# Kernel optimization log

Hardware: AMD Instinct MI355X
Metric: run time of the kernel (lower is better)

Reference implementation:

```python
import jax, jax.numpy as jnp
import numpy as np

B, D_IN, M, D_MEM = 65536, 64, 2048, 64


def setup_inputs() -> dict:
    key = jax.random.key(0)
    k = jax.random.split(key, 5)
    glorot = lambda kk, shape: jax.random.uniform(
        kk, shape, jnp.float32,
        -jnp.sqrt(6.0 / (shape[0] + shape[1])), jnp.sqrt(6.0 / (shape[0] + shape[1])))
    return {
        "inputs": jax.random.normal(k[0], (B, D_IN), jnp.float32),
        "W_att": glorot(k[1], (D_IN, M)),
        "b_att": jnp.zeros((M,), jnp.float32),
        "W_write": glorot(k[2], (D_IN, D_MEM)),
        "b_write": jnp.zeros((D_MEM,), jnp.float32),
        "memory": glorot(k[3], (M, D_MEM)),
        "update_gate": jnp.full((M,), 0.5, jnp.float32),
    }


def reference(inputs, W_att, b_att, W_write, b_write, memory, update_gate):
    # Read attention: Dense(memory_size, softmax) -> [B, M]
    read_attention = jax.nn.softmax(inputs @ W_att + b_att, axis=-1)
    # Read: [B, M] @ [M, Dm] -> [B, Dm]
    read_vector = read_attention @ memory
    # Write candidate: Dense(memory_dim, tanh) -> [B, Dm]
    candidate_write = jnp.tanh(inputs @ W_write + b_write)
    aggregated_write = jnp.mean(candidate_write, axis=0)[None, :]  # [1, Dm]
    write_attention = jnp.mean(read_attention, axis=0)             # [M]
    update_weights = (write_attention * update_gate)[:, None]      # [M, 1]
    # Gated in-place memory update (returned as new state)
    new_memory = memory * (1.0 - update_weights) + update_weights * aggregated_write
    return read_vector, new_memory
```

## Files before the change

kernel.cpp:

```cpp
#include <hip/hip_runtime.h>
#include <hip/hip_bf16.h>

typedef unsigned int   u32;
typedef unsigned short u16;

typedef __bf16 bf16x8 __attribute__((ext_vector_type(8)));
typedef float  f32x4  __attribute__((ext_vector_type(4)));
typedef u32    u32x4  __attribute__((ext_vector_type(4)));

union Frag { u32x4 u; bf16x8 b; };

#define MFMA16 __builtin_amdgcn_mfma_f32_16x16x32_bf16

#define B_ROWS 65536
#define D_IN   64
#define M_SZ   2048
#define D_MEM  64

#define WT_OFF      0
#define MEMT_OFF    262144
#define WWT_OFF     524288
#define CSF_OFF     532480
#define AGF_OFF     540672
#define CSP_OFF     540928
#define AGP_OFF     8929536
#define WS_REQUIRED 9191680

#define L2E 1.4426950408889634f

__device__ __forceinline__ float bf2f(u16 h) { return __uint_as_float(((u32)h) << 16); }
__device__ __forceinline__ u16 f2bf(float f) {
    u32 u = __float_as_uint(f);
    return (u16)((u + 0x7FFFu + ((u >> 16) & 1u)) >> 16);
}
__device__ __forceinline__ u16 f2bf_fast(float f) {
    return (u16)((__float_as_uint(f) + 0x8000u) >> 16);
}
#if defined(__has_builtin) && __has_builtin(__builtin_amdgcn_exp2f)
__device__ __forceinline__ float exp2fast(float x) { return __builtin_amdgcn_exp2f(x); }
#else
__device__ __forceinline__ float exp2fast(float x) { return __expf(x * 0.6931471805599453f); }
#endif
__device__ __forceinline__ float tanh_fast(float x) {
    const float e = exp2fast(x * (2.0f * L2E));
    return 1.0f - 2.0f * __builtin_amdgcn_rcpf(e + 1.0f);
}
__device__ __forceinline__ bool detect_bf16(const void* ug) {
    return ((const u32*)ug)[0] == 0x3F003F00u;
}
__device__ __forceinline__ float load_elem(const void* p, size_t i, bool isbf) {
    return isbf ? bf2f(((const u16*)p)[i]) : ((const float*)p)[i];
}

__global__ void __launch_bounds__(256)
prep_kernel(const void* Watt, const void* mem_in, const void* Wwr, const void* ug,
            u16* Wt, u16* memT, u16* Wwt, float* CSF)
{
    const bool isbf = detect_bf16(ug);
    const int b = blockIdx.x;
    const int t = threadIdx.x;
    if (b == 65) {
        for (int i = t; i < 2112; i += 256) CSF[i] = 0.f;
        return;
    }
    __shared__ u16 tile[64][65];
    const void* src; u16* dst; int R, C, rb, cb;
    if (b < 32)      { src = Watt;   dst = Wt;   R = 64;   C = 2048; rb = 0;           cb = b * 64; }
    else if (b < 64) { src = mem_in; dst = memT; R = 2048; C = 64;   rb = (b-32) * 64; cb = 0;      }
    else             { src = Wwr;    dst = Wwt;  R = 64;   C = 64;   rb = 0;           cb = 0;      }

#pragma unroll
    for (int j = 0; j < 16; ++j) {
        int e = j * 256 + t;
        int r = e >> 6, c = e & 63;
        float v = load_elem(src, (size_t)(rb + r) * C + cb + c, isbf);
        tile[r][c] = f2bf(v);
    }
    __syncthreads();
#pragma unroll
    for (int j = 0; j < 16; ++j) {
        int e = j * 256 + t;
        int c2 = e >> 6, r2 = e & 63;
        dst[(size_t)(cb + c2) * R + rb + r2] = tile[r2][c2];
    }
}

__global__ void __launch_bounds__(256, 2)
main_kernel(const void* x_in, const void* batt_in, const void* bwrite_in,
            const u16* __restrict__ Wt, const u16* __restrict__ memT,
            const u16* __restrict__ Wwt, const void* ug,
            float* CSF, float* AGF, u16* cs_part, u16* ag_part,
            int use_part, void* out)
{
    const bool isbf = detect_bf16(ug);
    const int tid = threadIdx.x;
    const int lane = tid & 63, wave = tid >> 6;
    const int quad = lane >> 4, l4 = lane & 15;
    const int rowbase = blockIdx.x * 128;
    const int wrow = blockIdx.x * 4 + wave;

    __shared__ __align__(16) u16 WtL[2][64][72];
    __shared__ __align__(16) u16 MeL[2][64][72];
    __shared__ __align__(16) u16 P[4][32][72];
    __shared__ float battL[2048];

    {
        const int i0 = tid * 8;
#pragma unroll
        for (int j = 0; j < 8; ++j)
            battL[i0 + j] = load_elem(batt_in, i0 + j, isbf) * L2E;
    }

    const int srow = tid >> 2, sg = (tid & 3) * 16;
    auto stageWt = [&](int c, int b) {
        const u16* g = Wt + ((size_t)c * 64 + srow) * 64 + sg;
        u32x4 v0 = *(const u32x4*)g;
        u32x4 v1 = *(const u32x4*)(g + 8);
        *(u32x4*)&WtL[b][srow][sg]     = v0;
        *(u32x4*)&WtL[b][srow][sg + 8] = v1;
    };
    auto stageMe = [&](int c, int b) {
        const u16* g = memT + (size_t)srow * 2048 + c * 64 + sg;
        u32x4 v0 = *(const u32x4*)g;
        u32x4 v1 = *(const u32x4*)(g + 8);
        *(u32x4*)&MeL[b][srow][sg]     = v0;
        *(u32x4*)&MeL[b][srow][sg + 8] = v1;
    };

    Frag a[2][2];
#pragma unroll
    for (int rg = 0; rg < 2; ++rg) {
        const int arow = rowbase + wave * 32 + rg * 16 + l4;
        if (isbf) {
            const u16* xp = (const u16*)x_in + (size_t)arow * 64 + quad * 8;
            a[rg][0].u = *(const u32x4*)xp;
            a[rg][1].u = *(const u32x4*)(xp + 32);
        } else {
            const float* xp = (const float*)x_in + (size_t)arow * 64 + quad * 8;
#pragma unroll
            for (int j = 0; j < 8; ++j) {
                ((u16*)&a[rg][0])[j] = f2bf(xp[j]);
                ((u16*)&a[rg][1])[j] = f2bf(xp[32 + j]);
            }
        }
    }
    const f32x4 zf = {0.f, 0.f, 0.f, 0.f};

    stageWt(0, 0);

    float agout = 0.f;
    {
        f32x4 accW[4][2];
#pragma unroll
        for (int t = 0; t < 4; ++t) {
            const u16* bp = Wwt + (size_t)(t * 16 + l4) * 64 + quad * 8;
            Frag b0, b1; b0.u = *(const u32x4*)bp; b1.u = *(const u32x4*)(bp + 32);
#pragma unroll
            for (int rg = 0; rg < 2; ++rg) {
                accW[t][rg] = MFMA16(a[rg][0].b, b0.b, zf, 0, 0, 0);
                accW[t][rg] = MFMA16(a[rg][1].b, b1.b, accW[t][rg], 0, 0, 0);
            }
        }
#pragma unroll
        for (int t = 0; t < 4; ++t) {
            const float bw = load_elem(bwrite_in, t * 16 + l4, isbf);
            float s = 0.f;
#pragma unroll
            for (int rg = 0; rg < 2; ++rg)
#pragma unroll
                for (int i = 0; i < 4; ++i) s += tanh_fast(accW[t][rg][i] + bw);
            s += __shfl_xor(s, 16, 64);
            s += __shfl_xor(s, 32, 64);
            if (quad == t) agout = s;
        }
    }
    if (use_part) ag_part[wrow * 64 + lane] = f2bf(agout);
    else          atomicAdd(&AGF[lane], agout);

    __syncthreads();

    float lr[2][4] = {{0.f,0.f,0.f,0.f},{0.f,0.f,0.f,0.f}};
    for (int c = 0; c < 32; ++c) {
        const int buf = c & 1;
        if (c < 31) stageWt(c + 1, buf ^ 1);
        const int mbase = c * 64;
        Frag wb0[4], wb1[4]; float bl[4];
#pragma unroll
        for (int t = 0; t < 4; ++t) {
            wb0[t].u = *(const u32x4*)&WtL[buf][t * 16 + l4][quad * 8];
            wb1[t].u = *(const u32x4*)&WtL[buf][t * 16 + l4][32 + quad * 8];
            bl[t] = battL[mbase + t * 16 + l4];
        }
#pragma unroll
        for (int t = 0; t < 4; ++t)
#pragma unroll
            for (int rg = 0; rg < 2; ++rg) {
                f32x4 acc = MFMA16(a[rg][0].b, wb0[t].b, zf, 0, 0, 0);
                acc = MFMA16(a[rg][1].b, wb1[t].b, acc, 0, 0, 0);
#pragma unroll
                for (int i = 0; i < 4; ++i)
                    lr[rg][i] += exp2fast(fmaf(acc[i], L2E, bl[t]));
            }
        __syncthreads();
    }
#pragma unroll
    for (int rg = 0; rg < 2; ++rg)
#pragma unroll
        for (int i = 0; i < 4; ++i) {
            float v = lr[rg][i];
            v += __shfl_xor(v, 1, 64); v += __shfl_xor(v, 2, 64);
            v += __shfl_xor(v, 4, 64); v += __shfl_xor(v, 8, 64);
            lr[rg][i] = 1.f / v;
        }

    f32x4 oacc[2][4] = {{zf,zf,zf,zf},{zf,zf,zf,zf}};
    stageWt(0, 0); stageMe(0, 0);
    __syncthreads();
    for (int c = 0; c < 32; ++c) {
        const int buf = c & 1;
        if (c < 31) { stageWt(c + 1, buf ^ 1); stageMe(c + 1, buf ^ 1); }
        const int mbase = c * 64;
        Frag wb0[4], wb1[4], mb0[4], mb1[4]; float bl[4];
#pragma unroll
        for (int t = 0; t < 4; ++t) {
            wb0[t].u = *(const u32x4*)&WtL[buf][t * 16 + l4][quad * 8];
            wb1[t].u = *(const u32x4*)&WtL[buf][t * 16 + l4][32 + quad * 8];
            bl[t] = battL[mbase + t * 16 + l4];
            mb0[t].u = *(const u32x4*)&MeL[buf][t * 16 + l4][quad * 8];
            mb1[t].u = *(const u32x4*)&MeL[buf][t * 16 + l4][32 + quad * 8];
        }
        float cst[4];
#pragma unroll
        for (int t = 0; t < 4; ++t) {
            float cs = 0.f;
#pragma unroll
            for (int rg = 0; rg < 2; ++rg) {
                f32x4 acc = MFMA16(a[rg][0].b, wb0[t].b, zf, 0, 0, 0);
                acc = MFMA16(a[rg][1].b, wb1[t].b, acc, 0, 0, 0);
#pragma unroll
                for (int i = 0; i < 4; ++i) {
                    const float e = exp2fast(fmaf(acc[i], L2E, bl[t]));
                    const float p = e * lr[rg][i];
                    cs += p;
                    P[wave][rg * 16 + quad * 4 + i][t * 16 + l4] = f2bf_fast(p);
                }
            }
            cst[t] = cs;
        }
        Frag ap[2][2];
#pragma unroll
        for (int rg = 0; rg < 2; ++rg) {
            ap[rg][0].u = *(const u32x4*)&P[wave][rg * 16 + l4][quad * 8];
            ap[rg][1].u = *(const u32x4*)&P[wave][rg * 16 + l4][32 + quad * 8];
        }
#pragma unroll
        for (int dt = 0; dt < 4; ++dt)
#pragma unroll
            for (int rg = 0; rg < 2; ++rg) {
                oacc[rg][dt] = MFMA16(ap[rg][0].b, mb0[dt].b, oacc[rg][dt], 0, 0, 0);
                oacc[rg][dt] = MFMA16(ap[rg][1].b, mb1[dt].b, oacc[rg][dt], 0, 0, 0);
            }
        float csout = 0.f;
#pragma unroll
        for (int t = 0; t < 4; ++t) {
            float v = cst[t];
            v += __shfl_xor(v, 16, 64);
            v += __shfl_xor(v, 32, 64);
            if (quad == t) csout = v;
        }
        if (use_part) cs_part[(size_t)wrow * 2048 + mbase + lane] = f2bf(csout);
        else          atomicAdd(&CSF[mbase + lane], csout);
        __syncthreads();
    }

#pragma unroll
    for (int rg = 0; rg < 2; ++rg)
#pragma unroll
        for (int dt = 0; dt < 4; ++dt)
#pragma unroll
            for (int i = 0; i < 4; ++i) {
                const int gr = rowbase + wave * 32 + rg * 16 + quad * 4 + i;
                const int d = dt * 16 + l4;
                const float v = oacc[rg][dt][i];
                if (isbf) ((u16*)out)[(size_t)gr * 64 + d] = f2bf(v);
                else      ((float*)out)[(size_t)gr * 64 + d] = v;
            }
}

__global__ void __launch_bounds__(256)
reduce_kernel(const u16* __restrict__ cs_part, const u16* __restrict__ ag_part,
              float* CSF, float* AGF)
{
    const int b = blockIdx.x, t = threadIdx.x;
    if (b < 64) {
        const int m = (b & 7) * 256 + t;
        const int w0 = (b >> 3) * 256;
        float s = 0.f;
        for (int k = 0; k < 256; ++k) s += bf2f(cs_part[(size_t)(w0 + k) * 2048 + m]);
        atomicAdd(&CSF[m], s);
    } else if (t < 64) {
        const int w0 = (b - 64) * 512;
        float s = 0.f;
        for (int k = 0; k < 512; ++k) s += bf2f(ag_part[(w0 + k) * 64 + t]);
        atomicAdd(&AGF[t], s);
    }
}

__global__ void __launch_bounds__(256)
finalize_kernel(const void* mem_in, const void* ug,
                const float* __restrict__ CSF, const float* __restrict__ AGF,
                void* out)
{
    const bool isbf = detect_bf16(ug);
    const int idx = blockIdx.x * 256 + threadIdx.x;
    const int m = idx >> 6, d = idx & 63;
    const float wa  = CSF[m] * (1.f / 65536.f);
    const float agg = AGF[d] * (1.f / 65536.f);
    const float uw  = wa * load_elem(ug, m, isbf);
    const float mv  = load_elem(mem_in, idx, isbf);
    const float nm  = mv * (1.f - uw) + uw * agg;
    if (isbf) ((u16*)out)[(size_t)4194304 + idx] = f2bf(nm);
    else      ((float*)out)[(size_t)4194304 + idx] = nm;
}

extern "C" void kernel_launch(void* const* d_in, const int* in_sizes, int n_in,
                              void* d_out, int out_size, void* d_ws, size_t ws_size,
                              hipStream_t stream)
{
    (void)in_sizes; (void)n_in; (void)out_size;
    const void* x    = d_in[0];
    const void* Watt = d_in[1];
    const void* batt = d_in[2];
    const void* Wwr  = d_in[3];
    const void* bwr  = d_in[4];
    const void* mem  = d_in[5];
    const void* ug   = d_in[6];

    char* ws = (char*)d_ws;
    u16*   Wt      = (u16*)(ws + WT_OFF);
    u16*   memT    = (u16*)(ws + MEMT_OFF);
    u16*   Wwt     = (u16*)(ws + WWT_OFF);
    float* CSF     = (float*)(ws + CSF_OFF);
    float* AGF     = (float*)(ws + AGF_OFF);
    u16*   cs_part = (u16*)(ws + CSP_OFF);
    u16*   ag_part = (u16*)(ws + AGP_OFF);
    const int use_part = (ws_size >= (size_t)WS_REQUIRED) ? 1 : 0;

    prep_kernel<<<66, 256, 0, stream>>>(Watt, mem, Wwr, ug, Wt, memT, Wwt, CSF);
    main_kernel<<<512, 256, 0, stream>>>(x, batt, bwr, Wt, memT, Wwt, ug,
                                         CSF, AGF, cs_part, ag_part,
                                         use_part, d_out);
    if (use_part)
        reduce_kernel<<<68, 256, 0, stream>>>(cs_part, ag_part, CSF, AGF);
    finalize_kernel<<<512, 256, 0, stream>>>(mem, ug, CSF, AGF, d_out);
}
```

Baseline: 204.3 us.

## Keep softmax probabilities in registers via transposed MFMA and permlane swaps

Swaps the MFMA operand order so score tiles come out transposed, with each lane holding four consecutive M columns for one row. Probabilities are packed to bf16 with v_cvt_pk_bf16_f32 and rearranged into B-operand fragments with permlane32/16 swaps, so the per-wave shared-memory P buffer and its store/load round trip go away. Column sums now use DPP row reductions plus a select tree, and the final output is written with vector stores. This removes LDS traffic and bank conflicts, at the cost of more cross-lane ops and reliance on gfx950-specific instructions.

```diff
diff --git a/kernel.cpp b/kernel.cpp
--- a/kernel.cpp
+++ b/kernel.cpp
@@ -7,6 +7,7 @@
 typedef __bf16 bf16x8 __attribute__((ext_vector_type(8)));
 typedef float  f32x4  __attribute__((ext_vector_type(4)));
 typedef u32    u32x4  __attribute__((ext_vector_type(4)));
+typedef u32    u32x2  __attribute__((ext_vector_type(2)));
 
 union Frag { u32x4 u; bf16x8 b; };
 
@@ -33,9 +34,6 @@
     u32 u = __float_as_uint(f);
     return (u16)((u + 0x7FFFu + ((u >> 16) & 1u)) >> 16);
 }
-__device__ __forceinline__ u16 f2bf_fast(float f) {
-    return (u16)((__float_as_uint(f) + 0x8000u) >> 16);
-}
 #if defined(__has_builtin) && __has_builtin(__builtin_amdgcn_exp2f)
 __device__ __forceinline__ float exp2fast(float x) { return __builtin_amdgcn_exp2f(x); }
 #else
@@ -50,6 +48,42 @@
 }
 __device__ __forceinline__ float load_elem(const void* p, size_t i, bool isbf) {
     return isbf ? bf2f(((const u16*)p)[i]) : ((const float*)p)[i];
+}
+
+__device__ __forceinline__ u32 cvtpk_bf16(float lo, float hi) {
+    u32 r;
+    asm("v_cvt_pk_bf16_f32 %0, %1, %2" : "=v"(r) : "v"(lo), "v"(hi));
+    return r;
+}
+#if defined(__has_builtin) && __has_builtin(__builtin_amdgcn_permlane32_swap) && \
+    __has_builtin(__builtin_amdgcn_permlane16_swap)
+__device__ __forceinline__ void pl32swap(u32& a, u32& b) {
+    u32x2 r = __builtin_amdgcn_permlane32_swap(a, b, false, false);
+    a = r[0]; b = r[1];
+}
+__device__ __forceinline__ void pl16swap(u32& a, u32& b) {
+    u32x2 r = __builtin_amdgcn_permlane16_swap(a, b, false, false);
+    a = r[0]; b = r[1];
+}
+#else
+__device__ __forceinline__ void pl32swap(u32& a, u32& b) {
+    asm("v_permlane32_swap_b32 %0, %1" : "+v"(a), "+v"(b));
+}
+__device__ __forceinline__ void pl16swap(u32& a, u32& b) {
+    asm("v_permlane16_swap_b32 %0, %1" : "+v"(a), "+v"(b));
+}
+#endif
+template<int CTRL>
+__device__ __forceinline__ float rotadd(float v) {
+    int x = __builtin_amdgcn_update_dpp(0, __float_as_int(v), CTRL, 0xF, 0xF, false);
+    return v + __int_as_float(x);
+}
+__device__ __forceinline__ float rowsum16(float v) {
+    v = rotadd<0x128>(v);
+    v = rotadd<0x124>(v);
+    v = rotadd<0x122>(v);
+    v = rotadd<0x121>(v);
+    return v;
 }
 
 __global__ void __launch_bounds__(256)
@@ -101,8 +135,7 @@
 
     __shared__ __align__(16) u16 WtL[2][64][72];
     __shared__ __align__(16) u16 MeL[2][64][72];
-    __shared__ __align__(16) u16 P[4][32][72];
-    __shared__ float battL[2048];
+    __shared__ __align__(16) float battL[2048];
 
     {
         const int i0 = tid * 8;
@@ -179,112 +212,124 @@
 
     __syncthreads();
 
-    float lr[2][4] = {{0.f,0.f,0.f,0.f},{0.f,0.f,0.f,0.f}};
+    float lsum[2] = {0.f, 0.f};
     for (int c = 0; c < 32; ++c) {
         const int buf = c & 1;
         if (c < 31) stageWt(c + 1, buf ^ 1);
         const int mbase = c * 64;
-        Frag wb0[4], wb1[4]; float bl[4];
+        Frag wb0[4], wb1[4]; f32x4 blv[4];
 #pragma unroll
         for (int t = 0; t < 4; ++t) {
             wb0[t].u = *(const u32x4*)&WtL[buf][t * 16 + l4][quad * 8];
             wb1[t].u = *(const u32x4*)&WtL[buf][t * 16 + l4][32 + quad * 8];
-            bl[t] = battL[mbase + t * 16 + l4];
+            blv[t] = *(const f32x4*)&battL[mbase + t * 16 + quad * 4];
         }
 #pragma unroll
         for (int t = 0; t < 4; ++t)
 #pragma unroll
             for (int rg = 0; rg < 2; ++rg) {
-                f32x4 acc = MFMA16(a[rg][0].b, wb0[t].b, zf, 0, 0, 0);
-                acc = MFMA16(a[rg][1].b, wb1[t].b, acc, 0, 0, 0);
+                f32x4 acc = MFMA16(wb0[t].b, a[rg][0].b, zf, 0, 0, 0);
+                acc = MFMA16(wb1[t].b, a[rg][1].b, acc, 0, 0, 0);
 #pragma unroll
                 for (int i = 0; i < 4; ++i)
-                    lr[rg][i] += exp2fast(fmaf(acc[i], L2E, bl[t]));
+                    lsum[rg] += exp2fast(fmaf(acc[i], L2E, blv[t][i]));
             }
         __syncthreads();
     }
-#pragma unroll
-    for (int rg = 0; rg < 2; ++rg)
-#pragma unroll
-        for (int i = 0; i < 4; ++i) {
-            float v = lr[rg][i];
-            v += __shfl_xor(v, 1, 64); v += __shfl_xor(v, 2, 64);
-            v += __shfl_xor(v, 4, 64); v += __shfl_xor(v, 8, 64);
-            lr[rg][i] = 1.f / v;
-        }
-
-    f32x4 oacc[2][4] = {{zf,zf,zf,zf},{zf,zf,zf,zf}};
+    float invl[2];
+#pragma unroll
+    for (int rg = 0; rg < 2; ++rg) {
+        float v = lsum[rg];
+        v += __shfl_xor(v, 16, 64);
+        v += __shfl_xor(v, 32, 64);
+        invl[rg] = 1.f / v;
+    }
+
+    f32x4 oaccT[2][4] = {{zf,zf,zf,zf},{zf,zf,zf,zf}};
     stageWt(0, 0); stageMe(0, 0);
     __syncthreads();
+    const bool sb0 = (l4 & 1), sb1 = (l4 & 2), sb2 = (l4 & 4), sb3 = (l4 & 8);
     for (int c = 0; c < 32; ++c) {
         const int buf = c & 1;
         if (c < 31) { stageWt(c + 1, buf ^ 1); stageMe(c + 1, buf ^ 1); }
         const int mbase = c * 64;
-        Frag wb0[4], wb1[4], mb0[4], mb1[4]; float bl[4];
+        Frag wb0[4], wb1[4], mb0[4], mb1[4]; f32x4 blv[4];
 #pragma unroll
         for (int t = 0; t < 4; ++t) {
             wb0[t].u = *(const u32x4*)&WtL[buf][t * 16 + l4][quad * 8];
             wb1[t].u = *(const u32x4*)&WtL[buf][t * 16 + l4][32 + quad * 8];
-            bl[t] = battL[mbase + t * 16 + l4];
             mb0[t].u = *(const u32x4*)&MeL[buf][t * 16 + l4][quad * 8];
             mb1[t].u = *(const u32x4*)&MeL[buf][t * 16 + l4][32 + quad * 8];
-        }
-        float cst[4];
-#pragma unroll
-        for (int t = 0; t < 4; ++t) {
-            float cs = 0.f;
+            blv[t] = *(const f32x4*)&battL[mbase + t * 16 + quad * 4];
+        }
+        u32 P0[2][4], P1[2][4];
+        float c16[16];
+#pragma unroll
+        for (int j = 0; j < 16; ++j) c16[j] = 0.f;
+#pragma unroll
+        for (int t = 0; t < 4; ++t)
 #pragma unroll
             for (int rg = 0; rg < 2; ++rg) {
-                f32x4 acc = MFMA16(a[rg][0].b, wb0[t].b, zf, 0, 0, 0);
-                acc = MFMA16(a[rg][1].b, wb1[t].b, acc, 0, 0, 0);
-#pragma unroll
-                for (int i = 0; i < 4; ++i) {
-                    const float e = exp2fast(fmaf(acc[i], L2E, bl[t]));
-                    const float p = e * lr[rg][i];
-                    cs += p;
-                    P[wave][rg * 16 + quad * 4 + i][t * 16 + l4] = f2bf_fast(p);
+                f32x4 acc = MFMA16(wb0[t].b, a[rg][0].b, zf, 0, 0, 0);
+                acc = MFMA16(wb1[t].b, a[rg][1].b, acc, 0, 0, 0);
+                const float p0 = exp2fast(fmaf(acc[0], L2E, blv[t][0])) * invl[rg];
+                const float p1 = exp2fast(fmaf(acc[1], L2E, blv[t][1])) * invl[rg];
+                const float p2 = exp2fast(fmaf(acc[2], L2E, blv[t][2])) * invl[rg];
+                const float p3 = exp2fast(fmaf(acc[3], L2E, blv[t][3])) * invl[rg];
+                c16[t * 4 + 0] += p0; c16[t * 4 + 1] += p1;
+                c16[t * 4 + 2] += p2; c16[t * 4 + 3] += p3;
+                P0[rg][t] = cvtpk_bf16(p0, p1);
+                P1[rg][t] = cvtpk_bf16(p2, p3);
+            }
+#pragma unroll
+        for (int rg = 0; rg < 2; ++rg)
+#pragma unroll
+            for (int cc = 0; cc < 2; ++cc) {
+                u32 b0 = P0[rg][2 * cc], b2 = P0[rg][2 * cc + 1];
+                u32 b1 = P1[rg][2 * cc], b3 = P1[rg][2 * cc + 1];
+                pl32swap(b0, b2); pl16swap(b0, b2);
+                pl32swap(b1, b3); pl16swap(b1, b3);
+                Frag bf; bf.u = (u32x4){b0, b1, b2, b3};
+#pragma unroll
+                for (int dt = 0; dt < 4; ++dt) {
+                    if (cc == 0)
+                        oaccT[rg][dt] = MFMA16(mb0[dt].b, bf.b, oaccT[rg][dt], 0, 0, 0);
+                    else
+                        oaccT[rg][dt] = MFMA16(mb1[dt].b, bf.b, oaccT[rg][dt], 0, 0, 0);
                 }
             }
-            cst[t] = cs;
-        }
-        Frag ap[2][2];
-#pragma unroll
-        for (int rg = 0; rg < 2; ++rg) {
-            ap[rg][0].u = *(const u32x4*)&P[wave][rg * 16 + l4][quad * 8];
-            ap[rg][1].u = *(const u32x4*)&P[wave][rg * 16 + l4][32 + quad * 8];
-        }
-#pragma unroll
-        for (int dt = 0; dt < 4; ++dt)
-#pragma unroll
-            for (int rg = 0; rg < 2; ++rg) {
-                oacc[rg][dt] = MFMA16(ap[rg][0].b, mb0[dt].b, oacc[rg][dt], 0, 0, 0);
-                oacc[rg][dt] = MFMA16(ap[rg][1].b, mb1[dt].b, oacc[rg][dt], 0, 0, 0);
-            }
-        float csout = 0.f;
-#pragma unroll
-        for (int t = 0; t < 4; ++t) {
-            float v = cst[t];
-            v += __shfl_xor(v, 16, 64);
-            v += __shfl_xor(v, 32, 64);
-            if (quad == t) csout = v;
-        }
-        if (use_part) cs_part[(size_t)wrow * 2048 + mbase + lane] = f2bf(csout);
-        else          atomicAdd(&CSF[mbase + lane], csout);
+#pragma unroll
+        for (int j = 0; j < 16; ++j) c16[j] = rowsum16(c16[j]);
+        float s8[8], s4[4], s2[2];
+#pragma unroll
+        for (int k = 0; k < 8; ++k) s8[k] = sb0 ? c16[2 * k + 1] : c16[2 * k];
+#pragma unroll
+        for (int k = 0; k < 4; ++k) s4[k] = sb1 ? s8[2 * k + 1] : s8[2 * k];
+        s2[0] = sb2 ? s4[1] : s4[0];
+        s2[1] = sb2 ? s4[3] : s4[2];
+        const float csv = sb3 ? s2[1] : s2[0];
+        const int mout = mbase + (l4 >> 2) * 16 + quad * 4 + (l4 & 3);
+        if (use_part) cs_part[(size_t)wrow * 2048 + mout] = f2bf(csv);
+        else          atomicAdd(&CSF[mout], csv);
         __syncthreads();
     }
 
 #pragma unroll
     for (int rg = 0; rg < 2; ++rg)
 #pragma unroll
-        for (int dt = 0; dt < 4; ++dt)
-#pragma unroll
-            for (int i = 0; i < 4; ++i) {
-                const int gr = rowbase + wave * 32 + rg * 16 + quad * 4 + i;
-                const int d = dt * 16 + l4;
-                const float v = oacc[rg][dt][i];
-                if (isbf) ((u16*)out)[(size_t)gr * 64 + d] = f2bf(v);
-                else      ((float*)out)[(size_t)gr * 64 + d] = v;
-            }
+        for (int dt = 0; dt < 4; ++dt) {
+            const int gr = rowbase + wave * 32 + rg * 16 + l4;
+            const int d0 = dt * 16 + quad * 4;
+            const f32x4 o = oaccT[rg][dt];
+            if (isbf) {
+                u32x2 w;
+                w.x = cvtpk_bf16(o[0], o[1]);
+                w.y = cvtpk_bf16(o[2], o[3]);
+                *(u32x2*)&((u16*)out)[(size_t)gr * 64 + d0] = w;
+            } else {
+                *(f32x4*)&((float*)out)[(size_t)gr * 64 + d0] = o;
+            }
+        }
 }
 
 __global__ void __launch_bounds__(256)
```

New measurement: 242.3 us. +18.6%, slower.
